# Optimization experiments

Hardware: AMD Instinct MI355X
Metric: run time of the kernel (lower is better)

## Reference

```python
import jax, jax.numpy as jnp
import numpy as np

B = 64
SEG = 4096
N = B * SEG
C = 512
MID = 4 * C
EPS = 1e-5


def setup_inputs() -> dict:
    key = jax.random.key(0)
    ks = jax.random.split(key, 8)
    s_in = 1.0 / np.sqrt(C)
    s_mid = 1.0 / np.sqrt(MID)
    return {
        "x2": jax.random.normal(ks[0], (N, C), dtype=jnp.float32),
        "npoint": jnp.full((B,), SEG, dtype=jnp.int64) if jax.config.jax_enable_x64 else jnp.full((B,), SEG, dtype=jnp.int32),
        "W1a": jax.random.normal(ks[1], (C, MID), dtype=jnp.float32) * s_in,
        "g1a": jnp.ones((MID,), dtype=jnp.float32),
        "b1a": jnp.zeros((MID,), dtype=jnp.float32),
        "W2a": jax.random.normal(ks[2], (MID, C), dtype=jnp.float32) * s_mid,
        "W1b": jax.random.normal(ks[3], (C, MID), dtype=jnp.float32) * s_in,
        "g1b": jnp.ones((MID,), dtype=jnp.float32),
        "b1b": jnp.zeros((MID,), dtype=jnp.float32),
        "W2b": jax.random.normal(ks[4], (MID, C), dtype=jnp.float32) * s_mid,
    }


def _bn(h, g, b):
    # training-mode BatchNorm1d over the segment (batch) axis
    m = jnp.mean(h, axis=0)
    v = jnp.var(h, axis=0)
    return (h - m) * jax.lax.rsqrt(v + EPS) * g + b


def reference(x2, npoint, W1a, g1a, b1a, W2a, W1b, g1b, b1b, W2b):
    n = x2.shape[0]
    b = npoint.shape[0]
    # segment id for every point: seg[j] = i  iff  cumsum(npoint)[i-1] <= j < cumsum(npoint)[i]
    cum = jnp.cumsum(npoint)
    seg = jnp.searchsorted(cum, jnp.arange(n), side="right")  # [N]
    counts = npoint.astype(x2.dtype)  # [B]
    # per-segment mean  [B, C]
    mean_f = jax.ops.segment_sum(x2, seg, num_segments=b) / counts[:, None]
    # fc branch: Linear -> BN -> ReLU -> Linear -> ReLU
    ha = jax.nn.relu(_bn(mean_f @ W1a, g1a, b1a))
    out_mean = jax.nn.relu(ha @ W2a)  # [B, C]
    # fc1 branch + sigmoid
    hb = jax.nn.relu(_bn(mean_f @ W1b, g1b, b1b))
    out_w = jax.nn.sigmoid(jax.nn.relu(hb @ W2b))  # [B, C]
    # broadcast per-segment stats back to points and combine
    return out_w[seg] * x2 * 0.5 + x2 * 0.75 + out_mean[seg]
```

## Files before the change

### kernel.cpp

```cpp
#include <hip/hip_runtime.h>
#include <hip/hip_bf16.h>
#include <math.h>

#define NB    64
#define CD    512
#define CV    128
#define MIDD  2048
#define RS2   32
#define EPSV  1e-5f
#define FPT   8
#define FROWS 16

typedef float fx4 __attribute__((ext_vector_type(4)));

__device__ __forceinline__ float wave_sum64(float x) {
    #pragma unroll
    for (int o = 32; o; o >>= 1) x += __shfl_xor(x, o, 64);
    return x;
}

__device__ __forceinline__ int seg_search(const int* __restrict__ cum, int row) {
    int lo = 0, hi = NB - 1;
    while (lo < hi) {
        int mid = (lo + hi) >> 1;
        if (cum[mid] > row) hi = mid; else lo = mid + 1;
    }
    return lo;
}

__global__ __launch_bounds__(256) void k_partial(const float* __restrict__ x2,
                          const int* __restrict__ npoint,
                          float* __restrict__ P) {
    int bx = blockIdx.x;
    int b  = bx >> 5;
    int rs = bx & (RS2 - 1);
    int t = threadIdx.x;
    int lane = t & 63;
    int np = npoint[lane];
    int ps = np;
    #pragma unroll
    for (int o = 1; o < 64; o <<= 1) {
        int v = __shfl_up(ps, o, 64);
        if (lane >= o) ps += v;
    }
    int len    = __shfl(np, b, 64);
    int startb = __shfl(ps, b, 64) - len;

    int chunk = (len + RS2 - 1) / RS2;
    int r0 = rs * chunk;
    int r1 = min(r0 + chunk, len);

    int c = t & 127;
    int p = t >> 7;
    const fx4* xv = (const fx4*)x2;
    fx4 a0 = 0.f, a1 = 0.f, a2 = 0.f, a3 = 0.f;
    int r = r0 + p;
    for (; r + 6 < r1; r += 8) {
        fx4 v0 = xv[(size_t)(startb + r)     * CV + c];
        fx4 v1 = xv[(size_t)(startb + r + 2) * CV + c];
        fx4 v2 = xv[(size_t)(startb + r + 4) * CV + c];
        fx4 v3 = xv[(size_t)(startb + r + 6) * CV + c];
        a0 += v0; a1 += v1; a2 += v2; a3 += v3;
    }
    for (; r < r1; r += 2)
        a0 += xv[(size_t)(startb + r) * CV + c];

    __shared__ fx4 red[256];
    red[t] = (a0 + a1) + (a2 + a3);
    __syncthreads();
    if (t < 128)
        ((fx4*)P)[(size_t)bx * CV + t] = red[t] + red[t + 128];
}

__global__ __launch_bounds__(512) void k_mean(const float* __restrict__ P,
                       const int* __restrict__ npoint,
                       float* __restrict__ mean_t,
                       int* __restrict__ cum) {
    __shared__ fx4 red[4][CV];
    int b = blockIdx.x;
    int t = threadIdx.x;
    int cv = t & 127;
    int rq = t >> 7;
    const fx4* Pv = (const fx4*)P;
    fx4 acc = 0.f;
    #pragma unroll 8
    for (int rs = rq * 8; rs < rq * 8 + 8; ++rs)
        acc += Pv[((size_t)(b * RS2 + rs)) * CV + cv];
    red[rq][cv] = acc;
    __syncthreads();
    if (t < 128) {
        fx4 s = (red[0][t] + red[1][t]) + (red[2][t] + red[3][t]);
        float inv = 1.0f / (float)npoint[b];
        int c = 4 * t;
        mean_t[(size_t)(c + 0) * NB + b] = s.x * inv;
        mean_t[(size_t)(c + 1) * NB + b] = s.y * inv;
        mean_t[(size_t)(c + 2) * NB + b] = s.z * inv;
        mean_t[(size_t)(c + 3) * NB + b] = s.w * inv;
    }
    if (t == 0) {
        int s = 0;
        for (int i = 0; i <= b; ++i) s += npoint[i];
        cum[b] = s;
    }
}

__global__ __launch_bounds__(512) void k_fc1(const float* __restrict__ mean_t,
                                             const float* __restrict__ W1a,
                                             const float* __restrict__ g1a,
                                             const float* __restrict__ b1a,
                                             const float* __restrict__ W1b,
                                             const float* __restrict__ g1b,
                                             const float* __restrict__ b1b,
                                             const int* __restrict__ cum,
                                             unsigned char* __restrict__ segtab,
                                             float* __restrict__ h_t) {
    __shared__ float red[8][64][9];
    int bx = blockIdx.x;
    int branch = bx >> 8;
    int cg = bx & 255;
    int c0 = cg * 8;
    const float* W1 = branch ? W1b : W1a;
    const float* g  = branch ? g1b : g1a;
    const float* bb = branch ? b1b : b1a;
    int t = threadIdx.x;

    int gid = bx * 512 + t;
    if (gid < 16384) {
        int r0 = gid * FROWS;
        int lo = seg_search(cum, r0);
        int hi = seg_search(cum, r0 + FROWS - 1);
        segtab[gid] = (lo == hi) ? (unsigned char)lo : (unsigned char)255;
    }

    int lane = t & 63;
    int w = t >> 6;
    float acc[8];
    #pragma unroll
    for (int i = 0; i < 8; ++i) acc[i] = 0.f;
    int k0 = w * 64;
    for (int k = k0; k < k0 + 64; ++k) {
        float mval = mean_t[(size_t)k * NB + lane];
        const float4* wr = (const float4*)(W1 + (size_t)k * MIDD + c0);
        float4 w0 = wr[0], w1 = wr[1];
        acc[0] += mval * w0.x; acc[1] += mval * w0.y;
        acc[2] += mval * w0.z; acc[3] += mval * w0.w;
        acc[4] += mval * w1.x; acc[5] += mval * w1.y;
        acc[6] += mval * w1.z; acc[7] += mval * w1.w;
    }
    #pragma unroll
    for (int i = 0; i < 8; ++i) red[w][lane][i] = acc[i];
    __syncthreads();
    float v = red[0][lane][w];
    #pragma unroll
    for (int ww = 1; ww < 8; ++ww) v += red[ww][lane][w];
    float s = wave_sum64(v);
    float m = s * (1.0f / 64.0f);
    float d = v - m;
    float q = wave_sum64(d * d);
    float var = q * (1.0f / 64.0f);
    float val = fmaxf(d * rsqrtf(var + EPSV) * g[c0 + w] + bb[c0 + w], 0.0f);
    h_t[((size_t)branch * MIDD + c0 + w) * NB + lane] = val;
}

__global__ __launch_bounds__(512) void k_fc2(const float* __restrict__ h_t,
                                             const float* __restrict__ W2a,
                                             const float* __restrict__ W2b,
                                             float* __restrict__ out_mean,
                                             float* __restrict__ out_w) {
    __shared__ float red[8][64][5];
    int bx = blockIdx.x;
    int branch = bx >> 7;
    int cg = bx & 127;
    int c0 = cg * 4;
    const float* W2 = branch ? W2b : W2a;
    int t = threadIdx.x;
    int lane = t & 63;
    int w = t >> 6;
    float acc[4] = {0.f, 0.f, 0.f, 0.f};
    int k0 = w * 256;
    for (int k = k0; k < k0 + 256; ++k) {
        float hv = h_t[((size_t)branch * MIDD + k) * NB + lane];
        const float4* wr = (const float4*)(W2 + (size_t)k * CD + c0);
        float4 w0 = wr[0];
        acc[0] += hv * w0.x; acc[1] += hv * w0.y;
        acc[2] += hv * w0.z; acc[3] += hv * w0.w;
    }
    #pragma unroll
    for (int i = 0; i < 4; ++i) red[w][lane][i] = acc[i];
    __syncthreads();
    if (w < 4) {
        float v = red[0][lane][w];
        #pragma unroll
        for (int ww = 1; ww < 8; ++ww) v += red[ww][lane][w];
        float r = fmaxf(v, 0.0f);
        if (branch)
            out_w[(size_t)lane * CD + c0 + w] = 1.0f / (1.0f + expf(-r));
        else
            out_mean[(size_t)lane * CD + c0 + w] = r;
    }
}

__global__ __launch_bounds__(256) void k_final(const float* __restrict__ x2,
                        const int* __restrict__ cum,
                        const unsigned char* __restrict__ segtab,
                        const float* __restrict__ out_mean,
                        const float* __restrict__ out_w,
                        float* __restrict__ out) {
    int t = threadIdx.x;
    int bx = (int)gridDim.x - 1 - (int)blockIdx.x;
    size_t base = (size_t)bx << 11;
    int base_row = bx << 4;
    const fx4* xv = (const fx4*)x2;
    const fx4* wv = (const fx4*)out_w;
    const fx4* mv = (const fx4*)out_mean;
    fx4* ov = (fx4*)out;

    int stab = segtab[bx];

    fx4 xs[FPT];
    #pragma unroll
    for (int k = 0; k < FPT; ++k)
        xs[k] = xv[base + ((size_t)k << 8) + t];

    int colv = t & 127;

    if (stab != 255) {
        fx4 ww = wv[(size_t)stab * CV + colv];
        fx4 mm = mv[(size_t)stab * CV + colv];
        fx4 a = ww * 0.5f + 0.75f;
        #pragma unroll
        for (int k = 0; k < FPT; ++k) {
            fx4 o = xs[k] * a + mm;
            __builtin_nontemporal_store(o, &ov[base + ((size_t)k << 8) + t]);
        }
    } else {
        #pragma unroll
        for (int k = 0; k < FPT; ++k) {
            int row = base_row + ((k * 256 + t) >> 7);
            int seg = seg_search(cum, row);
            fx4 ww = wv[(size_t)seg * CV + colv];
            fx4 mm = mv[(size_t)seg * CV + colv];
            fx4 o = xs[k] * (ww * 0.5f + 0.75f) + mm;
            __builtin_nontemporal_store(o, &ov[base + ((size_t)k << 8) + t]);
        }
    }
}

extern "C" void kernel_launch(void* const* d_in, const int* in_sizes, int n_in,
                              void* d_out, int out_size, void* d_ws, size_t ws_size,
                              hipStream_t stream) {
    const float* x2  = (const float*)d_in[0];
    const int*   npt = (const int*)d_in[1];
    const float* W1a = (const float*)d_in[2];
    const float* g1a = (const float*)d_in[3];
    const float* b1a = (const float*)d_in[4];
    const float* W2a = (const float*)d_in[5];
    const float* W1b = (const float*)d_in[6];
    const float* g1b = (const float*)d_in[7];
    const float* b1b = (const float*)d_in[8];
    const float* W2b = (const float*)d_in[9];
    float* out = (float*)d_out;

    const int N   = in_sizes[0] / CD;
    const int NC4 = (N * CD) / 4;
    const int NFB = NC4 / (256 * FPT);

    float* P      = out;
    float* mean_t = out + (size_t)NB * RS2 * CD;
    float* h_t    = mean_t + (size_t)NB * CD;
    int*   cum      = (int*)d_ws;
    float* out_mean = (float*)d_ws + 64;
    float* out_w    = out_mean + (size_t)NB * CD;
    unsigned char* segtab = (unsigned char*)(out_w + (size_t)NB * CD);

    k_partial<<<NB * RS2, 256, 0, stream>>>(x2, npt, P);
    k_mean<<<NB, 512, 0, stream>>>(P, npt, mean_t, cum);
    k_fc1<<<2 * (MIDD / 8), 512, 0, stream>>>(mean_t, W1a, g1a, b1a, W1b, g1b, b1b, cum, segtab, h_t);
    k_fc2<<<2 * (CD / 4), 512, 0, stream>>>(h_t, W2a, W2b, out_mean, out_w);
    k_final<<<NFB, 256, 0, stream>>>(x2, cum, segtab, out_mean, out_w, out);
}
```

Measured before the change: 349.3 us.

## Fuse all stages into one cooperative persistent kernel with grid syncs

Replaces the five-kernel pipeline (partial sums, mean, fc1, fc2, final combine) with a single cooperative kernel of 512 blocks that uses grid.sync between stages. Work per stage is redistributed to fit the fixed grid: 8 row slabs per segment instead of 32, fc1 over 4 waves with two output columns per wave, and fc2 over 2 columns per block. The final pass loops over 32 tiles per block and computes segment ids inline instead of reading a precomputed table. The aim is to remove kernel launch gaps and inter-kernel drain, at the cost of lower parallelism in the reduction and GEMV stages plus the overhead of grid-wide barriers. The old multi-kernel path is kept as a fallback if the cooperative launch fails.

```diff
diff --git a/kernel.cpp b/kernel.cpp
--- a/kernel.cpp
+++ b/kernel.cpp
@@ -1,17 +1,21 @@
 #include <hip/hip_runtime.h>
 #include <hip/hip_bf16.h>
+#include <hip/hip_cooperative_groups.h>
 #include <math.h>
 
 #define NB    64
 #define CD    512
 #define CV    128
 #define MIDD  2048
-#define RS2   32
 #define EPSV  1e-5f
 #define FPT   8
 #define FROWS 16
+#define RS2   32
+#define CSLAB 8
 
 typedef float fx4 __attribute__((ext_vector_type(4)));
+
+namespace cg = cooperative_groups;
 
 __device__ __forceinline__ float wave_sum64(float x) {
     #pragma unroll
@@ -26,6 +30,203 @@
         if (cum[mid] > row) hi = mid; else lo = mid + 1;
     }
     return lo;
+}
+
+__global__ __launch_bounds__(256, 4) void k_fused(
+        const float* __restrict__ x2, const int* __restrict__ npoint,
+        const float* __restrict__ W1a, const float* __restrict__ g1a,
+        const float* __restrict__ b1a, const float* __restrict__ W2a,
+        const float* __restrict__ W1b, const float* __restrict__ g1b,
+        const float* __restrict__ b1b, const float* __restrict__ W2b,
+        float* __restrict__ P, float* __restrict__ mean_t, float* __restrict__ h_t,
+        int* __restrict__ cum, float* __restrict__ out_mean, float* __restrict__ out_w,
+        float* __restrict__ out) {
+    cg::grid_group grid = cg::this_grid();
+    __shared__ float smem[2304];
+
+    const int bx = blockIdx.x;
+    const int t  = threadIdx.x;
+    const int lane = t & 63;
+
+    {
+        int b  = bx >> 3;
+        int rs = bx & (CSLAB - 1);
+        int np = npoint[lane];
+        int ps = np;
+        #pragma unroll
+        for (int o = 1; o < 64; o <<= 1) {
+            int v = __shfl_up(ps, o, 64);
+            if (lane >= o) ps += v;
+        }
+        int len    = __shfl(np, b, 64);
+        int startb = __shfl(ps, b, 64) - len;
+        int chunk = (len + CSLAB - 1) / CSLAB;
+        int r0 = rs * chunk;
+        int r1 = min(r0 + chunk, len);
+
+        int c = t & 127;
+        int p = t >> 7;
+        const fx4* xv = (const fx4*)x2;
+        fx4 a0 = 0.f, a1 = 0.f, a2 = 0.f, a3 = 0.f;
+        int r = r0 + p;
+        for (; r + 6 < r1; r += 8) {
+            fx4 v0 = xv[(size_t)(startb + r)     * CV + c];
+            fx4 v1 = xv[(size_t)(startb + r + 2) * CV + c];
+            fx4 v2 = xv[(size_t)(startb + r + 4) * CV + c];
+            fx4 v3 = xv[(size_t)(startb + r + 6) * CV + c];
+            a0 += v0; a1 += v1; a2 += v2; a3 += v3;
+        }
+        for (; r < r1; r += 2)
+            a0 += xv[(size_t)(startb + r) * CV + c];
+
+        fx4* red = (fx4*)smem;
+        red[t] = (a0 + a1) + (a2 + a3);
+        __syncthreads();
+        if (t < 128)
+            ((fx4*)P)[(size_t)bx * CV + t] = red[t] + red[t + 128];
+        __syncthreads();
+    }
+    grid.sync();
+
+    if (bx < NB) {
+        int b = bx;
+        int cv = t & 127;
+        int h  = t >> 7;
+        const fx4* Pv = (const fx4*)P;
+        fx4 acc = 0.f;
+        #pragma unroll 4
+        for (int rs = h * 4; rs < h * 4 + 4; ++rs)
+            acc += Pv[((size_t)(b * CSLAB + rs)) * CV + cv];
+        fx4* red = (fx4*)smem;
+        red[t] = acc;
+        __syncthreads();
+        if (t < 128) {
+            fx4 s = red[t] + red[t + 128];
+            float inv = 1.0f / (float)npoint[b];
+            int c = 4 * t;
+            mean_t[(size_t)(c + 0) * NB + b] = s.x * inv;
+            mean_t[(size_t)(c + 1) * NB + b] = s.y * inv;
+            mean_t[(size_t)(c + 2) * NB + b] = s.z * inv;
+            mean_t[(size_t)(c + 3) * NB + b] = s.w * inv;
+        }
+        if (t == 0) {
+            int s = 0;
+            for (int i = 0; i <= b; ++i) s += npoint[i];
+            cum[b] = s;
+        }
+    }
+    grid.sync();
+
+    {
+        int branch = bx >> 8;
+        int c0 = (bx & 255) * 8;
+        const float* W1 = branch ? W1b : W1a;
+        const float* g  = branch ? g1b : g1a;
+        const float* bb = branch ? b1b : b1a;
+        int w = t >> 6;
+        float acc[8];
+        #pragma unroll
+        for (int i = 0; i < 8; ++i) acc[i] = 0.f;
+        int k0 = w * 128;
+        for (int k = k0; k < k0 + 128; ++k) {
+            float mval = mean_t[(size_t)k * NB + lane];
+            const float4* wr = (const float4*)(W1 + (size_t)k * MIDD + c0);
+            float4 w0 = wr[0], w1 = wr[1];
+            acc[0] += mval * w0.x; acc[1] += mval * w0.y;
+            acc[2] += mval * w0.z; acc[3] += mval * w0.w;
+            acc[4] += mval * w1.x; acc[5] += mval * w1.y;
+            acc[6] += mval * w1.z; acc[7] += mval * w1.w;
+        }
+        float* red = smem;
+        #pragma unroll
+        for (int i = 0; i < 8; ++i) red[(w * 64 + lane) * 9 + i] = acc[i];
+        __syncthreads();
+        #pragma unroll
+        for (int pass = 0; pass < 2; ++pass) {
+            int col = w + pass * 4;
+            float v = red[(0 * 64 + lane) * 9 + col];
+            #pragma unroll
+            for (int ww = 1; ww < 4; ++ww) v += red[(ww * 64 + lane) * 9 + col];
+            float s = wave_sum64(v);
+            float m = s * (1.0f / 64.0f);
+            float d = v - m;
+            float q = wave_sum64(d * d);
+            float var = q * (1.0f / 64.0f);
+            float val = fmaxf(d * rsqrtf(var + EPSV) * g[c0 + col] + bb[c0 + col], 0.0f);
+            h_t[((size_t)branch * MIDD + c0 + col) * NB + lane] = val;
+        }
+        __syncthreads();
+    }
+    grid.sync();
+
+    {
+        int branch = bx >> 8;
+        int c0 = (bx & 255) * 2;
+        const float* W2 = branch ? W2b : W2a;
+        int w = t >> 6;
+        float acc0 = 0.f, acc1 = 0.f;
+        int k0 = w * 512;
+        for (int k = k0; k < k0 + 512; ++k) {
+            float hv = h_t[((size_t)branch * MIDD + k) * NB + lane];
+            acc0 += hv * W2[(size_t)k * CD + c0];
+            acc1 += hv * W2[(size_t)k * CD + c0 + 1];
+        }
+        float* red = smem;
+        red[(w * 64 + lane) * 2 + 0] = acc0;
+        red[(w * 64 + lane) * 2 + 1] = acc1;
+        __syncthreads();
+        if (w < 2) {
+            float v = red[(0 * 64 + lane) * 2 + w];
+            #pragma unroll
+            for (int ww = 1; ww < 4; ++ww) v += red[(ww * 64 + lane) * 2 + w];
+            float r = fmaxf(v, 0.0f);
+            if (branch)
+                out_w[(size_t)lane * CD + c0 + w] = 1.0f / (1.0f + expf(-r));
+            else
+                out_mean[(size_t)lane * CD + c0 + w] = r;
+        }
+        __syncthreads();
+    }
+    grid.sync();
+
+    {
+        int R0 = bx << 9;
+        const fx4* xv = (const fx4*)x2;
+        const fx4* wv = (const fx4*)out_w;
+        const fx4* mv = (const fx4*)out_mean;
+        fx4* ov = (fx4*)out;
+        int colv = t & 127;
+        for (int j = 31; j >= 0; --j) {
+            int base_row = R0 + j * 16;
+            size_t base = (size_t)base_row << 7;
+            fx4 xs[FPT];
+            #pragma unroll
+            for (int k = 0; k < FPT; ++k)
+                xs[k] = xv[base + ((size_t)k << 8) + t];
+            int seg_lo = seg_search(cum, base_row);
+            int seg_hi = seg_search(cum, base_row + 15);
+            if (seg_lo == seg_hi) {
+                fx4 ww = wv[(size_t)seg_lo * CV + colv];
+                fx4 mm = mv[(size_t)seg_lo * CV + colv];
+                fx4 a = ww * 0.5f + 0.75f;
+                #pragma unroll
+                for (int k = 0; k < FPT; ++k) {
+                    fx4 o = xs[k] * a + mm;
+                    __builtin_nontemporal_store(o, &ov[base + ((size_t)k << 8) + t]);
+                }
+            } else {
+                #pragma unroll
+                for (int k = 0; k < FPT; ++k) {
+                    int row = base_row + ((k * 256 + t) >> 7);
+                    int seg = seg_search(cum, row);
+                    fx4 ww = wv[(size_t)seg * CV + colv];
+                    fx4 mm = mv[(size_t)seg * CV + colv];
+                    fx4 o = xs[k] * (ww * 0.5f + 0.75f) + mm;
+                    __builtin_nontemporal_store(o, &ov[base + ((size_t)k << 8) + t]);
+                }
+            }
+        }
+    }
 }
 
 __global__ __launch_bounds__(256) void k_partial(const float* __restrict__ x2,
@@ -45,11 +246,9 @@
     }
     int len    = __shfl(np, b, 64);
     int startb = __shfl(ps, b, 64) - len;
-
     int chunk = (len + RS2 - 1) / RS2;
     int r0 = rs * chunk;
     int r1 = min(r0 + chunk, len);
-
     int c = t & 127;
     int p = t >> 7;
     const fx4* xv = (const fx4*)x2;
@@ -64,7 +263,6 @@
     }
     for (; r < r1; r += 2)
         a0 += xv[(size_t)(startb + r) * CV + c];
-
     __shared__ fx4 red[256];
     red[t] = (a0 + a1) + (a2 + a3);
     __syncthreads();
@@ -117,13 +315,12 @@
     __shared__ float red[8][64][9];
     int bx = blockIdx.x;
     int branch = bx >> 8;
-    int cg = bx & 255;
-    int c0 = cg * 8;
+    int cg4 = bx & 255;
+    int c0 = cg4 * 8;
     const float* W1 = branch ? W1b : W1a;
     const float* g  = branch ? g1b : g1a;
     const float* bb = branch ? b1b : b1a;
     int t = threadIdx.x;
-
     int gid = bx * 512 + t;
     if (gid < 16384) {
         int r0 = gid * FROWS;
@@ -131,7 +328,6 @@
         int hi = seg_search(cum, r0 + FROWS - 1);
         segtab[gid] = (lo == hi) ? (unsigned char)lo : (unsigned char)255;
     }
-
     int lane = t & 63;
     int w = t >> 6;
     float acc[8];
@@ -170,8 +366,8 @@
     __shared__ float red[8][64][5];
     int bx = blockIdx.x;
     int branch = bx >> 7;
-    int cg = bx & 127;
-    int c0 = cg * 4;
+    int cg4 = bx & 127;
+    int c0 = cg4 * 4;
     const float* W2 = branch ? W2b : W2a;
     int t = threadIdx.x;
     int lane = t & 63;
@@ -214,16 +410,12 @@
     const fx4* wv = (const fx4*)out_w;
     const fx4* mv = (const fx4*)out_mean;
     fx4* ov = (fx4*)out;
-
     int stab = segtab[bx];
-
     fx4 xs[FPT];
     #pragma unroll
     for (int k = 0; k < FPT; ++k)
         xs[k] = xv[base + ((size_t)k << 8) + t];
-
     int colv = t & 127;
-
     if (stab != 255) {
         fx4 ww = wv[(size_t)stab * CV + colv];
         fx4 mm = mv[(size_t)stab * CV + colv];
@@ -265,17 +457,32 @@
     const int NC4 = (N * CD) / 4;
     const int NFB = NC4 / (256 * FPT);
 
-    float* P      = out;
-    float* mean_t = out + (size_t)NB * RS2 * CD;
-    float* h_t    = mean_t + (size_t)NB * CD;
+    float* Pc     = out;
+    float* mean_c = out + (size_t)NB * CSLAB * CD;
+    float* h_c    = mean_c + (size_t)NB * CD;
+    float* Pf     = out;
+    float* mean_f = out + (size_t)NB * RS2 * CD;
+    float* h_f    = mean_f + (size_t)NB * CD;
     int*   cum      = (int*)d_ws;
     float* out_mean = (float*)d_ws + 64;
     float* out_w    = out_mean + (size_t)NB * CD;
     unsigned char* segtab = (unsigned char*)(out_w + (size_t)NB * CD);
 
-    k_partial<<<NB * RS2, 256, 0, stream>>>(x2, npt, P);
-    k_mean<<<NB, 512, 0, stream>>>(P, npt, mean_t, cum);
-    k_fc1<<<2 * (MIDD / 8), 512, 0, stream>>>(mean_t, W1a, g1a, b1a, W1b, g1b, b1b, cum, segtab, h_t);
-    k_fc2<<<2 * (CD / 4), 512, 0, stream>>>(h_t, W2a, W2b, out_mean, out_w);
-    k_final<<<NFB, 256, 0, stream>>>(x2, cum, segtab, out_mean, out_w, out);
-}
+    void* args[] = {
+        (void*)&x2, (void*)&npt,
+        (void*)&W1a, (void*)&g1a, (void*)&b1a, (void*)&W2a,
+        (void*)&W1b, (void*)&g1b, (void*)&b1b, (void*)&W2b,
+        (void*)&Pc, (void*)&mean_c, (void*)&h_c,
+        (void*)&cum, (void*)&out_mean, (void*)&out_w, (void*)&out
+    };
+    hipError_t err = hipLaunchCooperativeKernel((const void*)k_fused,
+                                                dim3(NB * CSLAB), dim3(256),
+                                                args, 0, stream);
+    if (err != hipSuccess) {
+        k_partial<<<NB * RS2, 256, 0, stream>>>(x2, npt, Pf);
+        k_mean<<<NB, 512, 0, stream>>>(Pf, npt, mean_f, cum);
+        k_fc1<<<2 * (MIDD / 8), 512, 0, stream>>>(mean_f, W1a, g1a, b1a, W1b, g1b, b1b, cum, segtab, h_f);
+        k_fc2<<<2 * (CD / 4), 512, 0, stream>>>(h_f, W2a, W2b, out_mean, out_w);
+        k_final<<<NFB, 256, 0, stream>>>(x2, cum, segtab, out_mean, out_w, out);
+    }
+}
```

Result: slower. 602.6 us (+72.5%).
